# Optimization experiments

Measured on AMD Instinct MI355X. Metric: run time of the kernel, lower is better.

Reference implementation:

```python
import jax, jax.numpy as jnp
import numpy as np

LATENT = 256
C = 512            # channels == window_size
STEP = C // 2      # 256
N_SAMPLES = 32768
N_FRAMES = N_SAMPLES // STEP   # 128
IMP = 4096         # impulse samples
B, E = 4, 64
EPS = 1e-8


def unit_norm(x, axis=-1):
    return x / (jnp.linalg.norm(x, axis=axis, keepdims=True) + EPS)


def hamming(n):
    # torch.hamming_window default (periodic=True)
    return (0.54 - 0.46 * jnp.cos(2.0 * jnp.pi * jnp.arange(n) / n)).astype(jnp.float32)


def layer_norm(x, g, b):
    mu = x.mean(-1, keepdims=True)
    var = x.var(-1, keepdims=True)
    return (x - mu) / jnp.sqrt(var + 1e-5) * g + b


def mlp(x, Ws, bs, g, bt):
    # LinearOutputStack: 3 hidden (linear -> LayerNorm -> leaky_relu) + output linear
    for j in range(3):
        x = x @ Ws[j] + bs[j]
        x = layer_norm(x, g[j], bt[j])
        x = jax.nn.leaky_relu(x, 0.2)
    return x @ Ws[3] + bs[3]


def _forward(embedding, impulse, W_def, b_def,
             Ws_imp, bs_imp, g_imp, bt_imp,
             Ws_lat, bs_lat, g_lat, bt_lat,
             Ws_out, bs_out, g_out, bt_out,
             W_w, b_w, W_b, b_b, W_l, b_l):
    Bq, Eq, _ = embedding.shape
    # shape deformations: latent -> (C, n_frames), unit-normed over channel dim
    deform = (embedding @ W_def + b_def).reshape(Bq, Eq, C, N_FRAMES)
    deform = unit_norm(deform, axis=2)
    deform = deform.transpose(0, 1, 3, 2)           # (B,E,T,C)
    weights = deform @ W_w + b_w                    # (B,E,T,C)
    biases = deform @ W_b + b_b                     # (B,E,T,C)
    leak = 0.1 + jax.nn.sigmoid(deform @ W_l + b_l) * 0.98  # (B,E,T,1)

    # window the impulse: frames of size C with hop STEP
    padded = jnp.pad(impulse, ((0, 0), (0, 0), (0, STEP)))
    starts = jnp.arange(IMP // STEP) * STEP
    idx = starts[:, None] + jnp.arange(C)[None, :]
    windowed = padded[..., idx]                     # (B,E,16,C)
    norms = jnp.linalg.norm(windowed, axis=-1, keepdims=True)
    emb = mlp(windowed, Ws_imp, bs_imp, g_imp, bt_imp)
    emb = unit_norm(emb) * norms                    # (B,E,16,C)
    # pad with zeros to n_frames: adding zero == original i < n_impulse_frames guard
    emb_pad = jnp.pad(emb, ((0, 0), (0, 0), (0, N_FRAMES - emb.shape[2]), (0, 0)))

    ham = hamming(C)

    xs = (weights.transpose(2, 0, 1, 3),
          biases.transpose(2, 0, 1, 3),
          leak.transpose(2, 0, 1, 3),
          emb_pad.transpose(2, 0, 1, 3))

    def step(h, x):
        w, b, lk, e = x
        h = h + e
        cn = jnp.linalg.norm(h, axis=-1, keepdims=True)
        h = h * w + b
        h = unit_norm(h) * cn
        ol = mlp(h, Ws_lat, bs_lat, g_lat, bt_lat)
        ol = unit_norm(ol) * (cn * lk)
        on = jnp.linalg.norm(ol, axis=-1, keepdims=True)
        h = h - ol
        h = unit_norm(h) * (cn - on)
        of = mlp(ol, Ws_out, bs_out, g_out, bt_out)
        of = of * ham
        of = unit_norm(of) * on
        return h, of

    h0 = jnp.zeros((Bq, Eq, C), dtype=embedding.dtype)
    _, frames = jax.lax.scan(step, h0, xs)          # (T,B,E,C)
    frames = frames.transpose(1, 2, 0, 3)           # (B,E,T,C)

    # overlap-add at hop STEP, trim to n_samples
    L = (N_FRAMES - 1) * STEP + C
    oa_idx = jnp.arange(N_FRAMES)[:, None] * STEP + jnp.arange(C)[None, :]
    out = jnp.zeros((Bq, Eq, L), dtype=embedding.dtype)
    out = out.at[:, :, oa_idx].add(frames)
    return out[..., :N_SAMPLES]


def setup_inputs() -> dict:
    key = jax.random.key(0)
    ks = jax.random.split(key, 24)
    s = 0.02
    d = {
        'embedding': jax.random.normal(ks[0], (B, E, LATENT), jnp.float32),
        'impulse': jax.random.normal(ks[1], (B, E, IMP), jnp.float32),
        'W_def': jax.random.normal(ks[2], (LATENT, C * N_FRAMES), jnp.float32) * s,
        'b_def': jnp.zeros((C * N_FRAMES,), jnp.float32),
        'W_w': jax.random.normal(ks[3], (C, C), jnp.float32) * s,
        'b_w': jnp.zeros((C,), jnp.float32),
        'W_b': jax.random.normal(ks[4], (C, C), jnp.float32) * s,
        'b_b': jnp.zeros((C,), jnp.float32),
        'W_l': jax.random.normal(ks[5], (C, 1), jnp.float32) * s,
        'b_l': jnp.zeros((1,), jnp.float32),
    }
    for name, k in (('imp', ks[6]), ('lat', ks[7]), ('out', ks[8])):
        d['Ws_' + name] = jax.random.normal(k, (4, C, C), jnp.float32) * s
        d['bs_' + name] = jnp.zeros((4, C), jnp.float32)
        d['g_' + name] = jnp.ones((3, C), jnp.float32)
        d['bt_' + name] = jnp.zeros((3, C), jnp.float32)
    return d


def reference(embedding, impulse, W_def, b_def,
              Ws_imp, bs_imp, g_imp, bt_imp,
              Ws_lat, bs_lat, g_lat, bt_lat,
              Ws_out, bs_out, g_out, bt_out,
              W_w, b_w, W_b, b_b, W_l, b_l):
    return _forward(embedding, impulse, W_def, b_def,
                    Ws_imp, bs_imp, g_imp, bt_imp,
                    Ws_lat, bs_lat, g_lat, bt_lat,
                    Ws_out, bs_out, g_out, bt_out,
                    W_w, b_w, W_b, b_b, W_l, b_l)
```

## Files before the change

kernel.cpp:

```cpp
#include <hip/hip_runtime.h>
#include <math.h>

#define NB 4
#define NE 64
#define BE 256
#define LAT 256
#define NC 512
#define NT 128
#define NDEF 65536
#define NIMP 4096
#define NF 16
#define EPSN 1e-8f
#define SPB 4
#define NSCAN 64
#define NSAMP 32768

typedef unsigned short ushort8 __attribute__((ext_vector_type(8)));
typedef short short8v __attribute__((ext_vector_type(8)));
typedef float f32x4 __attribute__((ext_vector_type(4)));

__device__ __forceinline__ unsigned short f2bf(float f) {
  const unsigned u = __float_as_uint(f);
  return (unsigned short)((u + 0x7FFFu + ((u >> 16) & 1u)) >> 16);
}

__device__ __forceinline__ void bar_nodrain() {
  asm volatile("s_waitcnt lgkmcnt(0)" ::: "memory");
  __builtin_amdgcn_s_barrier();
  __builtin_amdgcn_sched_barrier(0);
}

template <int NR>
__device__ __forceinline__ void blk_reduce1(const float* v, float* out,
                                            float* red) {
  const int tid = threadIdx.x, wave = tid >> 6, lane = tid & 63;
  float s[NR];
#pragma unroll
  for (int i = 0; i < NR; ++i) s[i] = v[i];
#pragma unroll
  for (int off = 32; off; off >>= 1) {
#pragma unroll
    for (int i = 0; i < NR; ++i) s[i] += __shfl_down(s[i], off);
  }
  if (lane == 0) {
#pragma unroll
    for (int i = 0; i < NR; ++i) red[wave * NR + i] = s[i];
  }
  bar_nodrain();
#pragma unroll
  for (int i = 0; i < NR; ++i) {
    float a = 0.f;
#pragma unroll
    for (int w = 0; w < 8; ++w) a += red[w * NR + i];
    out[i] = a;
  }
}

__global__ __launch_bounds__(64) void k_cvt(const float* __restrict__ W,
                                            unsigned short* __restrict__ Wmf) {
  const int lane = threadIdx.x;
  const int gg = blockIdx.x;
  const int p = gg & 3;
  const int kt = (gg >> 2) & 15;
  const int wv = (gg >> 6) & 7;
  const int layer = gg >> 9;
  const int col = wv * 64 + p * 16 + (lane & 15);
  const int k0 = kt * 32 + (lane >> 4) * 8;
  ushort8 o;
#pragma unroll
  for (int j = 0; j < 8; ++j)
    o[j] = f2bf(W[((size_t)layer * NC + k0 + j) * NC + col]);
  *reinterpret_cast<ushort8*>(Wmf + ((size_t)gg * 64 + lane) * 8) = o;
}

__global__ __launch_bounds__(64) void k_cvt_def(
    const float* __restrict__ W, unsigned short* __restrict__ Wd) {
  const int lane = threadIdx.x;
  const int gg = blockIdx.x;
  const int p = gg & 3;
  const int kt = (gg >> 2) & 7;
  const int wv = (gg >> 5) & 7;
  const int nb = gg >> 8;
  const int col = nb * 512 + wv * 64 + p * 16 + (lane & 15);
  const int k0 = kt * 32 + (lane >> 4) * 8;
  ushort8 o;
#pragma unroll
  for (int j = 0; j < 8; ++j)
    o[j] = f2bf(W[(size_t)(k0 + j) * NDEF + col]);
  *reinterpret_cast<ushort8*>(Wd + ((size_t)gg * 64 + lane) * 8) = o;
}

__global__ __launch_bounds__(512) void k_deform(
    const float* __restrict__ emb, const unsigned short* __restrict__ Wd,
    const float* __restrict__ bd, float* __restrict__ deform) {
  __shared__ __align__(16) unsigned short A_lds[16 * LAT];
  const int tid = threadIdx.x;
  const int wave = tid >> 6, lane = tid & 63;
  const int nb = blockIdx.x;
  const int m0 = blockIdx.y * 16;
  {
    char* ab = (char*)A_lds;
#pragma unroll
    for (int rep = 0; rep < 8; ++rep) {
      const int idx = rep * 512 + tid;
      const int row = idx >> 8;
      const int k = idx & 255;
      *(unsigned short*)(ab + row * 512 + ((k * 2) ^ ((row & 7) << 4))) =
          f2bf(emb[(size_t)(m0 + row) * LAT + k]);
    }
  }
  __syncthreads();
  const int arow = lane & 15;
  const int kgrp = lane >> 4;
  const int r0 = kgrp * 4;
  const int abase = arow * 512;
  const int axor = (arow & 7) << 4;
  const int akoff = kgrp * 16;
  float bdv[4];
#pragma unroll
  for (int p = 0; p < 4; ++p)
    bdv[p] = bd[nb * 512 + wave * 64 + p * 16 + (lane & 15)];
  const unsigned short* wfrag =
      Wd + (size_t)(nb * 8 + wave) * 16384 + lane * 8;
  f32x4 acc[4];
#pragma unroll
  for (int p = 0; p < 4; ++p) acc[p] = (f32x4){0.f, 0.f, 0.f, 0.f};
#pragma unroll
  for (int kt = 0; kt < 8; ++kt) {
    const short8v a = *(const short8v*)((const char*)A_lds + abase +
                                        (((kt * 64) + akoff) ^ axor));
#pragma unroll
    for (int p = 0; p < 4; ++p) {
      const short8v b = *(const short8v*)(wfrag + (kt * 4 + p) * 512);
      acc[p] = __builtin_amdgcn_mfma_f32_16x16x32_bf16(a, b, acc[p], 0, 0, 0);
    }
  }
#pragma unroll
  for (int q = 0; q < 4; ++q) {
    const int row = r0 + q;
#pragma unroll
    for (int p = 0; p < 4; ++p) {
      const int col = nb * 512 + wave * 64 + p * 16 + (lane & 15);
      deform[(size_t)(m0 + row) * NDEF + col] = acc[p][q] + bdv[p];
    }
  }
}

__global__ __launch_bounds__(512) void k_wb(
    const float* __restrict__ deform, const unsigned short* __restrict__ Wmf2,
    const float* __restrict__ bw, const float* __restrict__ bb,
    const float* __restrict__ Wl, const float* __restrict__ bl,
    float* __restrict__ weights, float* __restrict__ biases,
    float* __restrict__ leak) {
  __shared__ float xs[16][NC + 1];
  __shared__ __align__(16) unsigned short A_lds[16 * NC];
  __shared__ float rno[16], lks[16];
  const int tid = threadIdx.x;
  const int wave = tid >> 6, lane = tid & 63;
  const int be = blockIdx.x >> 3;
  const int t0 = (blockIdx.x & 7) * 16;
  const float* dbase = deform + (size_t)be * NDEF;
#pragma unroll
  for (int rep = 0; rep < 16; ++rep) {
    const int idx = rep * 512 + tid;
    const int c = idx >> 4;
    const int f = idx & 15;
    xs[f][c] = dbase[(size_t)c * NT + t0 + f];
  }
  __syncthreads();
  for (int f = wave; f < 16; f += 8) {
    float s = 0.f;
#pragma unroll
    for (int j = 0; j < 8; ++j) {
      const float v = xs[f][lane + 64 * j];
      s = fmaf(v, v, s);
    }
#pragma unroll
    for (int off = 32; off; off >>= 1) s += __shfl_down(s, off);
    if (lane == 0) rno[f] = sqrtf(s);
  }
  __syncthreads();
  {
    char* ab = (char*)A_lds;
#pragma unroll
    for (int i = 0; i < 16; ++i) {
      const float xv = xs[i][tid] / (rno[i] + EPSN);
      xs[i][tid] = xv;
      *(unsigned short*)(ab + i * 1024 + ((tid * 2) ^ ((i & 7) << 4))) =
          f2bf(xv);
    }
  }
  __syncthreads();
  for (int f = wave; f < 16; f += 8) {
    float s = 0.f;
#pragma unroll
    for (int j = 0; j < 8; ++j)
      s = fmaf(xs[f][lane + 64 * j], Wl[lane + 64 * j], s);
#pragma unroll
    for (int off = 32; off; off >>= 1) s += __shfl_down(s, off);
    if (lane == 0) lks[f] = s;
  }
  __syncthreads();
  if (tid < 16) {
    const float v = lks[tid] + bl[0];
    leak[(size_t)be * NT + t0 + tid] = 0.1f + 0.98f / (1.f + expf(-v));
  }
  const int arow = lane & 15;
  const int kgrp = lane >> 4;
  const int r0 = kgrp * 4;
  const int abase = arow * (NC * 2);
  const int axor = (arow & 7) << 4;
  const int akoff = kgrp * 16;
  float bwv[4], bbv[4];
#pragma unroll
  for (int p = 0; p < 4; ++p) {
    const int cp = wave * 64 + p * 16 + (lane & 15);
    bwv[p] = bw[cp];
    bbv[p] = bb[cp];
  }
  const unsigned short* wfrag = Wmf2 + (size_t)wave * 32768 + lane * 8;
  f32x4 accw[4], accb[4];
#pragma unroll
  for (int p = 0; p < 4; ++p) {
    accw[p] = (f32x4){0.f, 0.f, 0.f, 0.f};
    accb[p] = (f32x4){0.f, 0.f, 0.f, 0.f};
  }
#pragma unroll
  for (int kt = 0; kt < 16; ++kt) {
    const short8v a = *(const short8v*)((const char*)A_lds + abase +
                                        (((kt * 64) + akoff) ^ axor));
#pragma unroll
    for (int p = 0; p < 4; ++p) {
      const short8v b0 = *(const short8v*)(wfrag + (kt * 4 + p) * 512);
      accw[p] = __builtin_amdgcn_mfma_f32_16x16x32_bf16(a, b0, accw[p], 0, 0, 0);
      const short8v b1 =
          *(const short8v*)(wfrag + (size_t)262144 + (kt * 4 + p) * 512);
      accb[p] = __builtin_amdgcn_mfma_f32_16x16x32_bf16(a, b1, accb[p], 0, 0, 0);
    }
  }
#pragma unroll
  for (int q = 0; q < 4; ++q) {
    const int row = r0 + q;
#pragma unroll
    for (int p = 0; p < 4; ++p) {
      const int cp = wave * 64 + p * 16 + (lane & 15);
      const size_t o = ((size_t)be * NT + t0 + row) * NC + cp;
      weights[o] = accw[p][q] + bwv[p];
      biases[o] = accb[p][q] + bbv[p];
    }
  }
}

__device__ __forceinline__ void tile_gemm16(const float (*xs)[NC],
                                            const float* __restrict__ W,
                                            int tid, float acc[16]) {
#pragma unroll
  for (int i = 0; i < 16; ++i) acc[i] = 0.f;
  for (int k = 0; k < NC; k += 4) {
    const float w0 = W[(size_t)(k + 0) * NC + tid];
    const float w1 = W[(size_t)(k + 1) * NC + tid];
    const float w2 = W[(size_t)(k + 2) * NC + tid];
    const float w3 = W[(size_t)(k + 3) * NC + tid];
#pragma unroll
    for (int i = 0; i < 16; ++i) {
      const float4 a = *reinterpret_cast<const float4*>(&xs[i][k]);
      acc[i] = fmaf(a.x, w0, acc[i]);
      acc[i] = fmaf(a.y, w1, acc[i]);
      acc[i] = fmaf(a.z, w2, acc[i]);
      acc[i] = fmaf(a.w, w3, acc[i]);
    }
  }
}

__device__ __forceinline__ void ln_leaky16(float (*xs)[NC],
                                           const float* __restrict__ g,
                                           const float* __restrict__ bt,
                                           int layer, int tid, float* mu_s,
                                           float* rs_s) {
  const int wave = tid >> 6, lane = tid & 63;
  for (int f = wave; f < 16; f += 8) {
    float s = 0.f, s2 = 0.f;
#pragma unroll
    for (int j = 0; j < 8; ++j) {
      const float v = xs[f][lane + 64 * j];
      s += v;
      s2 = fmaf(v, v, s2);
    }
#pragma unroll
    for (int off = 32; off; off >>= 1) {
      s += __shfl_down(s, off);
      s2 += __shfl_down(s2, off);
    }
    if (lane == 0) {
      const float mu = s * (1.f / NC);
      mu_s[f] = mu;
      rs_s[f] = rsqrtf(s2 * (1.f / NC) - mu * mu + 1e-5f);
    }
  }
  __syncthreads();
  const float gv = g[layer * NC + tid], btv = bt[layer * NC + tid];
#pragma unroll
  for (int i = 0; i < 16; ++i) {
    const float y = (xs[i][tid] - mu_s[i]) * rs_s[i] * gv + btv;
    xs[i][tid] = y > 0.f ? y : 0.2f * y;
  }
  __syncthreads();
}

__global__ __launch_bounds__(512) void k_imp(
    const float* __restrict__ impulse, const float* __restrict__ Ws,
    const float* __restrict__ bs, const float* __restrict__ g,
    const float* __restrict__ bt, float* __restrict__ embo) {
  __shared__ float xs[16][NC];
  __shared__ float wno[16], mu_s[16], rs_s[16], ono[16];
  const int tid = threadIdx.x;
  const int wave = tid >> 6, lane = tid & 63;
  const int be = blockIdx.x;
  const float* ib = impulse + (size_t)be * NIMP;
  for (int f = 0; f < 16; ++f) {
    const int s = f * 256 + tid;
    xs[f][tid] = (s < NIMP) ? ib[s] : 0.f;
  }
  __syncthreads();
  for (int f = wave; f < 16; f += 8) {
    float s = 0.f;
#pragma unroll
    for (int j = 0; j < 8; ++j) {
      const float v = xs[f][lane + 64 * j];
      s = fmaf(v, v, s);
    }
#pragma unroll
    for (int off = 32; off; off >>= 1) s += __shfl_down(s, off);
    if (lane == 0) wno[f] = sqrtf(s);
  }
  __syncthreads();
  float acc[16];
  for (int layer = 0; layer < 4; ++layer) {
    tile_gemm16(xs, Ws + (size_t)layer * NC * NC, tid, acc);
    __syncthreads();
    const float bv = bs[layer * NC + tid];
#pragma unroll
    for (int i = 0; i < 16; ++i) xs[i][tid] = acc[i] + bv;
    __syncthreads();
    if (layer < 3) ln_leaky16(xs, g, bt, layer, tid, mu_s, rs_s);
  }
  for (int f = wave; f < 16; f += 8) {
    float s = 0.f;
#pragma unroll
    for (int j = 0; j < 8; ++j) {
      const float v = xs[f][lane + 64 * j];
      s = fmaf(v, v, s);
    }
#pragma unroll
    for (int off = 32; off; off >>= 1) s += __shfl_down(s, off);
    if (lane == 0) ono[f] = sqrtf(s);
  }
  __syncthreads();
  for (int f = 0; f < 16; ++f)
    embo[((size_t)be * NF + f) * NC + tid] =
        xs[f][tid] / (ono[f] + EPSN) * wno[f];
}

__global__ __launch_bounds__(512) void k_scan(
    const float* __restrict__ weights, const float* __restrict__ biases,
    const float* __restrict__ leak, const float* __restrict__ embw,
    const unsigned short* __restrict__ Wmf, const float* __restrict__ bs,
    const float* __restrict__ g, const float* __restrict__ bt,
    float* __restrict__ olb, float* __restrict__ onb) {
  __shared__ __align__(16) unsigned short A_lds[16 * NC];
  __shared__ __align__(16) unsigned short B_lds[8][4][2048];
  __shared__ float ol_lds[SPB][NC];
  __shared__ float redA[64];
  __shared__ float redB[32];
  __shared__ float st1[8][SPB], st2[8][SPB];
  __shared__ float lk_lds[SPB][NT];

  const int tid = threadIdx.x;
  const int wave = tid >> 6, lane = tid & 63;
  const int seq0 = blockIdx.x * SPB;

  {
    const int r = tid >> 7, tt = tid & 127;
    lk_lds[r][tt] = leak[(size_t)(seq0 + r) * NT + tt];
  }
  {
    unsigned* z = (unsigned*)(A_lds + SPB * NC);
    for (int i = tid; i < (16 - SPB) * NC / 2; i += 512) z[i] = 0u;
  }

  const int arow = lane & 15;
  const int kgrp = lane >> 4;
  const int abase = arow * (NC * 2);
  const int axor = (arow & 7) << 4;
  const int akoff = kgrp * 16;
  const bool crow = (kgrp == 0);

  float bsv[4][4], gv[3][4], btv[3][4];
#pragma unroll
  for (int p = 0; p < 4; ++p) {
    const int cp = wave * 64 + p * 16 + (lane & 15);
#pragma unroll
    for (int l = 0; l < 4; ++l) bsv[l][p] = bs[l * NC + cp];
#pragma unroll
    for (int l = 0; l < 3; ++l) {
      gv[l][p] = g[l * NC + cp];
      btv[l][p] = bt[l * NC + cp];
    }
  }
  const unsigned short* wfrag = Wmf + (size_t)wave * 32768 + lane * 8;

  auto issue_chunk = [&](int cc) {
    const int layer = cc >> 4, kt = cc & 15, slot = cc & 3;
#pragma unroll
    for (int p = 0; p < 4; ++p) {
      __builtin_amdgcn_global_load_lds(
          (const unsigned int*)(wfrag + (size_t)layer * 262144 +
                                (kt * 4 + p) * 512),
          (unsigned int*)&B_lds[wave][slot][p * 512], 16, 0, 0);
    }
  };

  float wpre[SPB], bpre[SPB], epre[SPB];
#pragma unroll
  for (int r = 0; r < SPB; ++r) {
    const size_t o = ((size_t)(seq0 + r) * NT) * NC + tid;
    wpre[r] = weights[o];
    bpre[r] = biases[o];
    epre[r] = embw[((size_t)(seq0 + r) * NF) * NC + tid];
  }

  __syncthreads();

  issue_chunk(0);
  issue_chunk(1);
  issue_chunk(2);

  float h[SPB], cn[SPB];
#pragma unroll
  for (int r = 0; r < SPB; ++r) { h[r] = 0.f; cn[r] = 0.f; }

#pragma unroll 1
  for (int t = 0; t < NT; ++t) {
    float hw[SPB];
    if (t < NF) {
#pragma unroll
      for (int r = 0; r < SPB; ++r) h[r] += epre[r];
      float v8[8], s8[8];
#pragma unroll
      for (int r = 0; r < SPB; ++r) {
        hw[r] = fmaf(h[r], wpre[r], bpre[r]);
        v8[r] = h[r] * h[r];
        v8[SPB + r] = hw[r] * hw[r];
      }
      if (t + 1 < NF) {
#pragma unroll
        for (int r = 0; r < SPB; ++r)
          epre[r] = embw[((size_t)(seq0 + r) * NF + t + 1) * NC + tid];
      }
      if (t + 1 < NT) {
#pragma unroll
        for (int r = 0; r < SPB; ++r) {
          const size_t o = ((size_t)(seq0 + r) * NT + t + 1) * NC + tid;
          wpre[r] = weights[o];
          bpre[r] = biases[o];
        }
      }
      blk_reduce1<8>(v8, s8, redA);
#pragma unroll
      for (int r = 0; r < SPB; ++r) {
        cn[r] = sqrtf(s8[r]);
        h[r] = hw[r] * (cn[r] / (sqrtf(s8[SPB + r]) + EPSN));
      }
    } else {
      float v4[SPB], s4[SPB];
#pragma unroll
      for (int r = 0; r < SPB; ++r) {
        hw[r] = fmaf(h[r], wpre[r], bpre[r]);
        v4[r] = hw[r] * hw[r];
      }
      if (t + 1 < NT) {
#pragma unroll
        for (int r = 0; r < SPB; ++r) {
          const size_t o = ((size_t)(seq0 + r) * NT + t + 1) * NC + tid;
          wpre[r] = weights[o];
          bpre[r] = biases[o];
        }
      }
      blk_reduce1<SPB>(v4, s4, redA);
#pragma unroll
      for (int r = 0; r < SPB; ++r)
        h[r] = hw[r] * (cn[r] / (sqrtf(s4[r]) + EPSN));
    }
    {
      char* ab = (char*)A_lds;
#pragma unroll
      for (int r = 0; r < SPB; ++r)
        *(unsigned short*)(ab + r * 1024 + ((tid * 2) ^ ((r & 7) << 4))) =
            f2bf(h[r]);
    }
    bar_nodrain();

#pragma unroll 1
    for (int layer = 0; layer < 4; ++layer) {
      f32x4 acc[4];
#pragma unroll
      for (int p = 0; p < 4; ++p) acc[p] = (f32x4){0.f, 0.f, 0.f, 0.f};
#pragma unroll
      for (int kt = 0; kt < 16; ++kt) {
        asm volatile("s_waitcnt vmcnt(8)" ::: "memory");
        const short8v a = *(const short8v*)((const char*)A_lds + abase +
                                            (((kt * 64) + akoff) ^ axor));
        const int slot = kt & 3;
#pragma unroll
        for (int p = 0; p < 4; ++p) {
          const short8v b =
              *(const short8v*)((const char*)&B_lds[wave][slot][0] + p * 1024 +
                                lane * 16);
          acc[p] =
              __builtin_amdgcn_mfma_f32_16x16x32_bf16(a, b, acc[p], 0, 0, 0);
        }
        issue_chunk((layer * 16 + kt + 3) & 63);
      }

      if (layer < 3) {
        float s1[SPB], s2[SPB];
#pragma unroll
        for (int q = 0; q < SPB; ++q) { s1[q] = 0.f; s2[q] = 0.f; }
#pragma unroll
        for (int p = 0; p < 4; ++p) {
#pragma unroll
          for (int q = 0; q < SPB; ++q) {
            const float y = acc[p][q] + bsv[layer][p];
            acc[p][q] = y;
            s1[q] += y;
            s2[q] = fmaf(y, y, s2[q]);
          }
        }
#pragma unroll
        for (int off = 1; off < 16; off <<= 1) {
#pragma unroll
          for (int q = 0; q < SPB; ++q) {
            s1[q] += __shfl_xor(s1[q], off);
            s2[q] += __shfl_xor(s2[q], off);
          }
        }
        if (lane == 0) {
#pragma unroll
          for (int q = 0; q < SPB; ++q) {
            st1[wave][q] = s1[q];
            st2[wave][q] = s2[q];
          }
        }
        bar_nodrain();
        float mu[SPB], rs[SPB];
#pragma unroll
        for (int q = 0; q < SPB; ++q) {
          float a1 = 0.f, a2 = 0.f;
#pragma unroll
          for (int w = 0; w < 8; ++w) {
            a1 += st1[w][q];
            a2 += st2[w][q];
          }
          mu[q] = a1 * (1.f / NC);
          rs[q] = rsqrtf(a2 * (1.f / NC) - mu[q] * mu[q] + 1e-5f);
        }
        if (crow) {
          char* ab = (char*)A_lds;
#pragma unroll
          for (int q = 0; q < SPB; ++q) {
#pragma unroll
            for (int p = 0; p < 4; ++p) {
              float y = (acc[p][q] - mu[q]) * rs[q] * gv[layer][p] +
                        btv[layer][p];
              y = y > 0.f ? y : 0.2f * y;
              const int cp = wave * 64 + p * 16 + (lane & 15);
              *(unsigned short*)(ab + q * 1024 +
                                 ((cp * 2) ^ ((q & 7) << 4))) = f2bf(y);
            }
          }
        }
        bar_nodrain();
      } else {
        float s2[SPB];
#pragma unroll
        for (int q = 0; q < SPB; ++q) s2[q] = 0.f;
#pragma unroll
        for (int p = 0; p < 4; ++p) {
#pragma unroll
          for (int q = 0; q < SPB; ++q) {
            const float y = acc[p][q] + bsv[3][p];
            acc[p][q] = y;
            s2[q] = fmaf(y, y, s2[q]);
          }
        }
#pragma unroll
        for (int off = 1; off < 16; off <<= 1) {
#pragma unroll
          for (int q = 0; q < SPB; ++q) s2[q] += __shfl_xor(s2[q], off);
        }
        if (lane == 0) {
#pragma unroll
          for (int q = 0; q < SPB; ++q) st2[wave][q] = s2[q];
        }
        if (crow) {
#pragma unroll
          for (int q = 0; q < SPB; ++q) {
#pragma unroll
            for (int p = 0; p < 4; ++p)
              ol_lds[q][wave * 64 + p * 16 + (lane & 15)] = acc[p][q];
          }
        }
        bar_nodrain();
        float sc[SPB], on[SPB];
#pragma unroll
        for (int r = 0; r < SPB; ++r) {
          float a2 = 0.f;
#pragma unroll
          for (int w = 0; w < 8; ++w) a2 += st2[w][r];
          const float no = sqrtf(a2);
          sc[r] = cn[r] * lk_lds[r][t] / (no + EPSN);
          on[r] = no * sc[r];
        }
        if (tid < SPB) onb[(size_t)(seq0 + tid) * NT + t] = on[tid];
        float v4[SPB], s4[SPB];
#pragma unroll
        for (int r = 0; r < SPB; ++r) {
          const float olv = ol_lds[r][tid] * sc[r];
          olb[((size_t)(seq0 + r) * NT + t) * NC + tid] = olv;
          h[r] -= olv;
          v4[r] = h[r] * h[r];
        }
        blk_reduce1<SPB>(v4, s4, redB);
#pragma unroll
        for (int r = 0; r < SPB; ++r) {
          h[r] *= (cn[r] - on[r]) / (sqrtf(s4[r]) + EPSN);
          cn[r] = fabsf(cn[r] - on[r]);
        }
      }
    }
  }
}

__global__ __launch_bounds__(1024) void k_zero(float* __restrict__ out) {
  out[(size_t)blockIdx.x * 1024 + threadIdx.x] = 0.f;
}

__global__ __launch_bounds__(512) void k_out(
    const float* __restrict__ olb, const float* __restrict__ onb,
    const unsigned short* __restrict__ Wmf, const float* __restrict__ bs,
    const float* __restrict__ g, const float* __restrict__ bt,
    float* __restrict__ out) {
  __shared__ __align__(16) unsigned short A_lds[16 * NC];
  __shared__ float st1[8][16], st2[8][16];
  __shared__ float on_l[16];
  const int tid = threadIdx.x;
  const int wave = tid >> 6, lane = tid & 63;
  const int m0 = blockIdx.x * 16;
  const int arow = lane & 15;
  const int kgrp = lane >> 4;
  const int r0 = kgrp * 4;
  const int abase = arow * (NC * 2);
  const int axor = (arow & 7) << 4;
  const int akoff = kgrp * 16;

  float bsv[4][4], gv[3][4], btv[3][4], hamv[4];
#pragma unroll
  for (int p = 0; p < 4; ++p) {
    const int cp = wave * 64 + p * 16 + (lane & 15);
#pragma unroll
    for (int l = 0; l < 4; ++l) bsv[l][p] = bs[l * NC + cp];
#pragma unroll
    for (int l = 0; l < 3; ++l) {
      gv[l][p] = g[l * NC + cp];
      btv[l][p] = bt[l * NC + cp];
    }
    hamv[p] =
        0.54f - 0.46f * cosf(6.283185307179586f * (float)cp / (float)NC);
  }
  if (tid < 16) on_l[tid] = onb[m0 + tid];
  {
    char* ab = (char*)A_lds;
    for (int i = 0; i < 16; ++i) {
      const float v = olb[(size_t)(m0 + i) * NC + tid];
      *(unsigned short*)(ab + i * 1024 + ((tid * 2) ^ ((i & 7) << 4))) =
          f2bf(v);
    }
  }
  __syncthreads();

  const unsigned short* wfrag = Wmf + (size_t)wave * 32768 + lane * 8;

#pragma unroll 1
  for (int layer = 0; layer < 4; ++layer) {
    f32x4 acc[4];
#pragma unroll
    for (int p = 0; p < 4; ++p) acc[p] = (f32x4){0.f, 0.f, 0.f, 0.f};
#pragma unroll
    for (int kt = 0; kt < 16; ++kt) {
      const short8v a = *(const short8v*)((const char*)A_lds + abase +
                                          (((kt * 64) + akoff) ^ axor));
#pragma unroll
      for (int p = 0; p < 4; ++p) {
        const short8v b = *(const short8v*)(wfrag + (size_t)layer * 262144 +
                                            (kt * 4 + p) * 512);
        acc[p] = __builtin_amdgcn_mfma_f32_16x16x32_bf16(a, b, acc[p], 0, 0, 0);
      }
    }
    if (layer < 3) {
      float s1[4], s2[4];
#pragma unroll
      for (int q = 0; q < 4; ++q) { s1[q] = 0.f; s2[q] = 0.f; }
#pragma unroll
      for (int p = 0; p < 4; ++p) {
#pragma unroll
        for (int q = 0; q < 4; ++q) {
          const float y = acc[p][q] + bsv[layer][p];
          acc[p][q] = y;
          s1[q] += y;
          s2[q] = fmaf(y, y, s2[q]);
        }
      }
#pragma unroll
      for (int off = 1; off < 16; off <<= 1) {
#pragma unroll
        for (int q = 0; q < 4; ++q) {
          s1[q] += __shfl_xor(s1[q], off);
          s2[q] += __shfl_xor(s2[q], off);
        }
      }
      if ((lane & 15) == 0) {
#pragma unroll
        for (int q = 0; q < 4; ++q) {
          st1[wave][r0 + q] = s1[q];
          st2[wave][r0 + q] = s2[q];
        }
      }
      __syncthreads();
      char* ab = (char*)A_lds;
#pragma unroll
      for (int q = 0; q < 4; ++q) {
        const int row = r0 + q;
        float a1 = 0.f, a2 = 0.f;
#pragma unroll
        for (int w = 0; w < 8; ++w) {
          a1 += st1[w][row];
          a2 += st2[w][row];
        }
        const float mu = a1 * (1.f / NC);
        const float rs = rsqrtf(a2 * (1.f / NC) - mu * mu + 1e-5f);
#pragma unroll
        for (int p = 0; p < 4; ++p) {
          float y = (acc[p][q] - mu) * rs * gv[layer][p] + btv[layer][p];
          y = y > 0.f ? y : 0.2f * y;
          const int cp = wave * 64 + p * 16 + (lane & 15);
          *(unsigned short*)(ab + row * 1024 +
                             ((cp * 2) ^ ((row & 7) << 4))) = f2bf(y);
        }
      }
      __syncthreads();
    } else {
      float s2[4];
#pragma unroll
      for (int q = 0; q < 4; ++q) s2[q] = 0.f;
#pragma unroll
      for (int p = 0; p < 4; ++p) {
#pragma unroll
        for (int q = 0; q < 4; ++q) {
          float y = (acc[p][q] + bsv[3][p]) * hamv[p];
          acc[p][q] = y;
          s2[q] = fmaf(y, y, s2[q]);
        }
      }
#pragma unroll
      for (int off = 1; off < 16; off <<= 1) {
#pragma unroll
        for (int q = 0; q < 4; ++q) s2[q] += __shfl_xor(s2[q], off);
      }
      if ((lane & 15) == 0) {
#pragma unroll
        for (int q = 0; q < 4; ++q) st2[wave][r0 + q] = s2[q];
      }
      __syncthreads();
#pragma unroll
      for (int q = 0; q < 4; ++q) {
        const int row = r0 + q;
        const int gr = m0 + row;
        const int be = gr >> 7;
        const int tt = gr & 127;
        float a2 = 0.f;
#pragma unroll
        for (int w = 0; w < 8; ++w) a2 += st2[w][row];
        const float inv = on_l[row] / (sqrtf(a2) + EPSN);
#pragma unroll
        for (int p = 0; p < 4; ++p) {
          const int cp = wave * 64 + p * 16 + (lane & 15);
          const int s = tt * 256 + cp;
          if (s < NSAMP)
            atomicAdd(&out[(size_t)be * NSAMP + s], acc[p][q] * inv);
        }
      }
    }
  }
}

extern "C" void kernel_launch(void* const* d_in, const int* in_sizes, int n_in,
                              void* d_out, int out_size, void* d_ws,
                              size_t ws_size, hipStream_t stream) {
  const float* embedding = (const float*)d_in[0];
  const float* impulse = (const float*)d_in[1];
  const float* W_def = (const float*)d_in[2];
  const float* b_def = (const float*)d_in[3];
  const float* W_w = (const float*)d_in[4];
  const float* b_w = (const float*)d_in[5];
  const float* W_b = (const float*)d_in[6];
  const float* b_b = (const float*)d_in[7];
  const float* W_l = (const float*)d_in[8];
  const float* b_l = (const float*)d_in[9];
  const float* Ws_imp = (const float*)d_in[10];
  const float* bs_imp = (const float*)d_in[11];
  const float* g_imp = (const float*)d_in[12];
  const float* bt_imp = (const float*)d_in[13];
  const float* Ws_lat = (const float*)d_in[14];
  const float* bs_lat = (const float*)d_in[15];
  const float* g_lat = (const float*)d_in[16];
  const float* bt_lat = (const float*)d_in[17];
  const float* Ws_out = (const float*)d_in[18];
  const float* bs_out = (const float*)d_in[19];
  const float* g_out = (const float*)d_in[20];
  const float* bt_out = (const float*)d_in[21];
  float* out = (float*)d_out;

  float* ws = (float*)d_ws;
  float* deform = ws;
  float* weights = deform + 16777216;
  float* biases = weights + 16777216;
  float* leakb = biases + 16777216;
  float* embw = leakb + 32768;
  float* onb = embw + 2097152;
  unsigned short* wmf = (unsigned short*)(onb + 32768);
  unsigned short* wmf_out = wmf + 1048576;
  unsigned short* wmf_wb = wmf_out + 1048576;
  unsigned short* wmf_def = (unsigned short*)weights;
  float* olb = deform;

  k_cvt<<<2048, 64, 0, stream>>>(Ws_lat, wmf);
  k_cvt<<<2048, 64, 0, stream>>>(Ws_out, wmf_out);
  k_cvt<<<512, 64, 0, stream>>>(W_w, wmf_wb);
  k_cvt<<<512, 64, 0, stream>>>(W_b, wmf_wb + 262144);
  k_cvt_def<<<32768, 64, 0, stream>>>(W_def, wmf_def);
  k_deform<<<dim3(128, 16), 512, 0, stream>>>(embedding, wmf_def, b_def,
                                              deform);
  k_wb<<<2048, 512, 0, stream>>>(deform, wmf_wb, b_w, b_b, W_l, b_l,
                                 weights, biases, leakb);
  k_imp<<<256, 512, 0, stream>>>(impulse, Ws_imp, bs_imp, g_imp, bt_imp, embw);
  k_zero<<<(BE * NSAMP) / 1024, 1024, 0, stream>>>(out);
  k_scan<<<NSCAN, 512, 0, stream>>>(weights, biases, leakb, embw, wmf, bs_lat,
                                    g_lat, bt_lat, olb, onb);
  k_out<<<2048, 512, 0, stream>>>(olb, onb, wmf_out, bs_out, g_out, bt_out,
                                  out);
}
```

Measured before the change: 4.170 ms.

## Port impulse MLP kernel to bf16 MFMA with fused layernorm epilogue

Rewrites k_imp so its four 512x512 layers run on bf16 MFMA instructions, reading weights pre-converted into fragment layout by an extra k_cvt launch. Activations stay in a swizzled bf16 LDS tile between layers. Layernorm statistics are computed with shuffle reductions on the accumulators, and the final unit-norm is fused into the last layer's epilogue. This replaces the scalar fp32 FMA GEMM and its repeated global weight reads, at the cost of bf16 precision and an extra conversion kernel.

```diff
diff --git a/kernel.cpp b/kernel.cpp
--- a/kernel.cpp
+++ b/kernel.cpp
@@ -251,71 +251,36 @@
   }
 }
 
-__device__ __forceinline__ void tile_gemm16(const float (*xs)[NC],
-                                            const float* __restrict__ W,
-                                            int tid, float acc[16]) {
-#pragma unroll
-  for (int i = 0; i < 16; ++i) acc[i] = 0.f;
-  for (int k = 0; k < NC; k += 4) {
-    const float w0 = W[(size_t)(k + 0) * NC + tid];
-    const float w1 = W[(size_t)(k + 1) * NC + tid];
-    const float w2 = W[(size_t)(k + 2) * NC + tid];
-    const float w3 = W[(size_t)(k + 3) * NC + tid];
-#pragma unroll
-    for (int i = 0; i < 16; ++i) {
-      const float4 a = *reinterpret_cast<const float4*>(&xs[i][k]);
-      acc[i] = fmaf(a.x, w0, acc[i]);
-      acc[i] = fmaf(a.y, w1, acc[i]);
-      acc[i] = fmaf(a.z, w2, acc[i]);
-      acc[i] = fmaf(a.w, w3, acc[i]);
-    }
-  }
-}
-
-__device__ __forceinline__ void ln_leaky16(float (*xs)[NC],
-                                           const float* __restrict__ g,
-                                           const float* __restrict__ bt,
-                                           int layer, int tid, float* mu_s,
-                                           float* rs_s) {
-  const int wave = tid >> 6, lane = tid & 63;
-  for (int f = wave; f < 16; f += 8) {
-    float s = 0.f, s2 = 0.f;
-#pragma unroll
-    for (int j = 0; j < 8; ++j) {
-      const float v = xs[f][lane + 64 * j];
-      s += v;
-      s2 = fmaf(v, v, s2);
-    }
-#pragma unroll
-    for (int off = 32; off; off >>= 1) {
-      s += __shfl_down(s, off);
-      s2 += __shfl_down(s2, off);
-    }
-    if (lane == 0) {
-      const float mu = s * (1.f / NC);
-      mu_s[f] = mu;
-      rs_s[f] = rsqrtf(s2 * (1.f / NC) - mu * mu + 1e-5f);
-    }
-  }
-  __syncthreads();
-  const float gv = g[layer * NC + tid], btv = bt[layer * NC + tid];
-#pragma unroll
-  for (int i = 0; i < 16; ++i) {
-    const float y = (xs[i][tid] - mu_s[i]) * rs_s[i] * gv + btv;
-    xs[i][tid] = y > 0.f ? y : 0.2f * y;
-  }
-  __syncthreads();
-}
-
 __global__ __launch_bounds__(512) void k_imp(
-    const float* __restrict__ impulse, const float* __restrict__ Ws,
+    const float* __restrict__ impulse, const unsigned short* __restrict__ Wmf,
     const float* __restrict__ bs, const float* __restrict__ g,
     const float* __restrict__ bt, float* __restrict__ embo) {
   __shared__ float xs[16][NC];
-  __shared__ float wno[16], mu_s[16], rs_s[16], ono[16];
+  __shared__ __align__(16) unsigned short A_lds[16 * NC];
+  __shared__ float st1[8][16], st2[8][16];
+  __shared__ float wno[16];
   const int tid = threadIdx.x;
   const int wave = tid >> 6, lane = tid & 63;
   const int be = blockIdx.x;
+  const int arow = lane & 15;
+  const int kgrp = lane >> 4;
+  const int r0 = kgrp * 4;
+  const int abase = arow * (NC * 2);
+  const int axor = (arow & 7) << 4;
+  const int akoff = kgrp * 16;
+
+  float bsv[4][4], gv[3][4], btv[3][4];
+#pragma unroll
+  for (int p = 0; p < 4; ++p) {
+    const int cp = wave * 64 + p * 16 + (lane & 15);
+#pragma unroll
+    for (int l = 0; l < 4; ++l) bsv[l][p] = bs[l * NC + cp];
+#pragma unroll
+    for (int l = 0; l < 3; ++l) {
+      gv[l][p] = g[l * NC + cp];
+      btv[l][p] = bt[l * NC + cp];
+    }
+  }
   const float* ib = impulse + (size_t)be * NIMP;
   for (int f = 0; f < 16; ++f) {
     const int s = f * 256 + tid;
@@ -334,31 +299,123 @@
     if (lane == 0) wno[f] = sqrtf(s);
   }
   __syncthreads();
-  float acc[16];
+  {
+    char* ab = (char*)A_lds;
+#pragma unroll
+    for (int i = 0; i < 16; ++i)
+      *(unsigned short*)(ab + i * 1024 + ((tid * 2) ^ ((i & 7) << 4))) =
+          f2bf(xs[i][tid]);
+  }
+  __syncthreads();
+
+  const unsigned short* wfrag = Wmf + (size_t)wave * 32768 + lane * 8;
+
+#pragma unroll 1
   for (int layer = 0; layer < 4; ++layer) {
-    tile_gemm16(xs, Ws + (size_t)layer * NC * NC, tid, acc);
-    __syncthreads();
-    const float bv = bs[layer * NC + tid];
-#pragma unroll
-    for (int i = 0; i < 16; ++i) xs[i][tid] = acc[i] + bv;
-    __syncthreads();
-    if (layer < 3) ln_leaky16(xs, g, bt, layer, tid, mu_s, rs_s);
-  }
-  for (int f = wave; f < 16; f += 8) {
-    float s = 0.f;
-#pragma unroll
-    for (int j = 0; j < 8; ++j) {
-      const float v = xs[f][lane + 64 * j];
-      s = fmaf(v, v, s);
-    }
-#pragma unroll
-    for (int off = 32; off; off >>= 1) s += __shfl_down(s, off);
-    if (lane == 0) ono[f] = sqrtf(s);
-  }
-  __syncthreads();
-  for (int f = 0; f < 16; ++f)
-    embo[((size_t)be * NF + f) * NC + tid] =
-        xs[f][tid] / (ono[f] + EPSN) * wno[f];
+    f32x4 acc[4];
+#pragma unroll
+    for (int p = 0; p < 4; ++p) acc[p] = (f32x4){0.f, 0.f, 0.f, 0.f};
+#pragma unroll
+    for (int kt = 0; kt < 16; ++kt) {
+      const short8v a = *(const short8v*)((const char*)A_lds + abase +
+                                          (((kt * 64) + akoff) ^ axor));
+#pragma unroll
+      for (int p = 0; p < 4; ++p) {
+        const short8v b = *(const short8v*)(wfrag + (size_t)layer * 262144 +
+                                            (kt * 4 + p) * 512);
+        acc[p] = __builtin_amdgcn_mfma_f32_16x16x32_bf16(a, b, acc[p], 0, 0, 0);
+      }
+    }
+    if (layer < 3) {
+      float s1[4], s2[4];
+#pragma unroll
+      for (int q = 0; q < 4; ++q) { s1[q] = 0.f; s2[q] = 0.f; }
+#pragma unroll
+      for (int p = 0; p < 4; ++p) {
+#pragma unroll
+        for (int q = 0; q < 4; ++q) {
+          const float y = acc[p][q] + bsv[layer][p];
+          acc[p][q] = y;
+          s1[q] += y;
+          s2[q] = fmaf(y, y, s2[q]);
+        }
+      }
+#pragma unroll
+      for (int off = 1; off < 16; off <<= 1) {
+#pragma unroll
+        for (int q = 0; q < 4; ++q) {
+          s1[q] += __shfl_xor(s1[q], off);
+          s2[q] += __shfl_xor(s2[q], off);
+        }
+      }
+      if ((lane & 15) == 0) {
+#pragma unroll
+        for (int q = 0; q < 4; ++q) {
+          st1[wave][r0 + q] = s1[q];
+          st2[wave][r0 + q] = s2[q];
+        }
+      }
+      __syncthreads();
+      char* ab = (char*)A_lds;
+#pragma unroll
+      for (int q = 0; q < 4; ++q) {
+        const int row = r0 + q;
+        float a1 = 0.f, a2 = 0.f;
+#pragma unroll
+        for (int w = 0; w < 8; ++w) {
+          a1 += st1[w][row];
+          a2 += st2[w][row];
+        }
+        const float mu = a1 * (1.f / NC);
+        const float rs = rsqrtf(a2 * (1.f / NC) - mu * mu + 1e-5f);
+#pragma unroll
+        for (int p = 0; p < 4; ++p) {
+          float y = (acc[p][q] - mu) * rs * gv[layer][p] + btv[layer][p];
+          y = y > 0.f ? y : 0.2f * y;
+          const int cp = wave * 64 + p * 16 + (lane & 15);
+          *(unsigned short*)(ab + row * 1024 +
+                             ((cp * 2) ^ ((row & 7) << 4))) = f2bf(y);
+        }
+      }
+      __syncthreads();
+    } else {
+      float s2[4];
+#pragma unroll
+      for (int q = 0; q < 4; ++q) s2[q] = 0.f;
+#pragma unroll
+      for (int p = 0; p < 4; ++p) {
+#pragma unroll
+        for (int q = 0; q < 4; ++q) {
+          const float y = acc[p][q] + bsv[3][p];
+          acc[p][q] = y;
+          s2[q] = fmaf(y, y, s2[q]);
+        }
+      }
+#pragma unroll
+      for (int off = 1; off < 16; off <<= 1) {
+#pragma unroll
+        for (int q = 0; q < 4; ++q) s2[q] += __shfl_xor(s2[q], off);
+      }
+      if ((lane & 15) == 0) {
+#pragma unroll
+        for (int q = 0; q < 4; ++q) st2[wave][r0 + q] = s2[q];
+      }
+      __syncthreads();
+#pragma unroll
+      for (int q = 0; q < 4; ++q) {
+        const int row = r0 + q;
+        float a2 = 0.f;
+#pragma unroll
+        for (int w = 0; w < 8; ++w) a2 += st2[w][row];
+        const float inv = wno[row] / (sqrtf(a2) + EPSN);
+#pragma unroll
+        for (int p = 0; p < 4; ++p) {
+          const int cp = wave * 64 + p * 16 + (lane & 15);
+          embo[((size_t)be * NF + row) * NC + cp] = acc[p][q] * inv;
+        }
+      }
+    }
+  }
 }
 
 __global__ __launch_bounds__(512) void k_scan(
@@ -840,6 +897,7 @@
   unsigned short* wmf = (unsigned short*)(onb + 32768);
   unsigned short* wmf_out = wmf + 1048576;
   unsigned short* wmf_wb = wmf_out + 1048576;
+  unsigned short* wmf_imp = wmf_wb + 524288;
   unsigned short* wmf_def = (unsigned short*)weights;
   float* olb = deform;
 
@@ -847,12 +905,14 @@
   k_cvt<<<2048, 64, 0, stream>>>(Ws_out, wmf_out);
   k_cvt<<<512, 64, 0, stream>>>(W_w, wmf_wb);
   k_cvt<<<512, 64, 0, stream>>>(W_b, wmf_wb + 262144);
+  k_cvt<<<2048, 64, 0, stream>>>(Ws_imp, wmf_imp);
   k_cvt_def<<<32768, 64, 0, stream>>>(W_def, wmf_def);
   k_deform<<<dim3(128, 16), 512, 0, stream>>>(embedding, wmf_def, b_def,
                                               deform);
   k_wb<<<2048, 512, 0, stream>>>(deform, wmf_wb, b_w, b_b, W_l, b_l,
                                  weights, biases, leakb);
-  k_imp<<<256, 512, 0, stream>>>(impulse, Ws_imp, bs_imp, g_imp, bt_imp, embw);
+  k_imp<<<256, 512, 0, stream>>>(impulse, wmf_imp, bs_imp, g_imp, bt_imp,
+                                 embw);
   k_zero<<<(BE * NSAMP) / 1024, 1024, 0, stream>>>(out);
   k_scan<<<NSCAN, 512, 0, stream>>>(weights, biases, leakb, embw, wmf, bs_lat,
                                     g_lat, bt_lat, olb, onb);
```

Measured after the change: 4.014 ms. 3.7% less time.
